# Kernel optimization log

Measured on AMD Instinct MI355X. Metric: run time of the kernel, lower is better.

The kernel has to match this reference:

```python
import jax, jax.numpy as jnp
import numpy as np

N, E, IN, HID, HEADS, LAYERS, CLASSES = 50000, 800000, 256, 128, 4, 3, 2
DH = HID // HEADS
EPS = 1e-5


def _layernorm(h, g, b):
    mu = jnp.mean(h, axis=-1, keepdims=True)
    var = jnp.mean(jnp.square(h - mu), axis=-1, keepdims=True)
    return (h - mu) / jnp.sqrt(var + EPS) * g + b


def setup_inputs() -> dict:
    key = jax.random.key(0)
    ks = jax.random.split(key, 16)

    def w(k, shape, fan_in):
        return jax.random.normal(k, shape, dtype=jnp.float32) / np.sqrt(fan_in).astype(np.float32)

    inp = {}
    inp["x"] = jax.random.normal(ks[0], (N, IN), dtype=jnp.float32)
    inp["edge_index"] = jax.random.randint(ks[1], (2, E), 0, N, dtype=jnp.int32)
    inp["batch"] = jnp.zeros((N,), dtype=jnp.int32)  # single graph
    # feature extractor: Linear(IN,HID) -> ReLU -> Linear(HID,HID)
    inp["fe_w1"] = w(ks[2], (HID, IN), IN)
    inp["fe_b1"] = jnp.zeros((HID,), jnp.float32)
    inp["fe_w2"] = w(ks[3], (HID, HID), HID)
    inp["fe_b2"] = jnp.zeros((HID,), jnp.float32)
    inp["conv_w"] = w(ks[4], (LAYERS, HID, 2 * HID), 2 * HID)
    inp["conv_b"] = jnp.zeros((LAYERS, HID), jnp.float32)
    inp["ln_g"] = jnp.ones((LAYERS, HID), jnp.float32)
    inp["ln_b"] = jnp.zeros((LAYERS, HID), jnp.float32)
    # MultiheadAttention(HID, 4 heads): packed in_proj + out_proj
    inp["in_proj_w"] = w(ks[5], (3 * HID, HID), HID)
    inp["in_proj_b"] = jnp.zeros((3 * HID,), jnp.float32)
    inp["out_w"] = w(ks[6], (HID, HID), HID)
    inp["out_b"] = jnp.zeros((HID,), jnp.float32)
    # classifier: Linear(2*HID, HID) -> ReLU -> Linear(HID, CLASSES)
    inp["c_w1"] = w(ks[7], (HID, 2 * HID), 2 * HID)
    inp["c_b1"] = jnp.zeros((HID,), jnp.float32)
    inp["c_w2"] = w(ks[8], (CLASSES, HID), HID)
    inp["c_b2"] = jnp.zeros((CLASSES,), jnp.float32)
    return inp


def reference(x, edge_index, batch, fe_w1, fe_b1, fe_w2, fe_b2, conv_w, conv_b,
              ln_g, ln_b, in_proj_w, in_proj_b, out_w, out_b, c_w1, c_b1, c_w2, c_b2):
    # feature extractor (dropout inactive in eval mode)
    h = jax.nn.relu(x @ fe_w1.T + fe_b1) @ fe_w2.T + fe_b2  # [N, HID]
    row, col = edge_index[0], edge_index[1]
    for i in range(LAYERS):
        # scatter_add of source-node features onto destination nodes
        nbr = jax.ops.segment_sum(h[row], col, num_segments=N)  # [N, HID]
        hcat = jnp.concatenate([h, nbr], axis=-1)               # [N, 2*HID]
        h = _layernorm(hcat @ conv_w[i].T + conv_b[i], ln_g[i], ln_b[i])
        h = jax.nn.relu(h)
    # MultiheadAttention with h.unsqueeze(0) and batch_first=False:
    # seq_len = 1, batch = N -> softmax over a single key yields weight 1.
    qkv = h @ in_proj_w.T + in_proj_b                          # [N, 3*HID]
    q, k, v = jnp.split(qkv, 3, axis=-1)
    qh = q.reshape(N, HEADS, DH)
    kh = k.reshape(N, HEADS, DH)
    vh = v.reshape(N, HEADS, DH)
    scores = jnp.sum(qh * kh, axis=-1) / np.sqrt(DH).astype(np.float32)  # [N, H]
    wts = jax.nn.softmax(scores[..., None], axis=-1)           # [N, H, 1] == 1
    attn = wts * vh                                            # [N, H, DH]
    h_attn = attn.reshape(N, HID) @ out_w.T + out_b
    h = h + h_attn
    # global mean / max pool over (all-zero) batch ids
    counts = jax.ops.segment_sum(jnp.ones((N, 1), h.dtype), batch, num_segments=1)
    h_mean = jax.ops.segment_sum(h, batch, num_segments=1) / counts      # [1, HID]
    h_max = jax.ops.segment_max(h, batch, num_segments=1)                # [1, HID]
    g = jnp.concatenate([h_mean, h_max], axis=-1)                        # [1, 2*HID]
    return jax.nn.relu(g @ c_w1.T + c_b1) @ c_w2.T + c_b2                # [1, CLASSES]
```

## Files before the change

kernel.cpp:

```cpp
#include <hip/hip_runtime.h>

constexpr int HID = 128;
constexpr int SCHUNK = 1024;
constexpr int CPAD = 16;

typedef __attribute__((ext_vector_type(8))) short short8;
typedef __attribute__((ext_vector_type(8))) unsigned short us8;
typedef __attribute__((ext_vector_type(4))) unsigned short us4;
typedef __attribute__((ext_vector_type(4))) float f32x4;

__device__ __forceinline__ unsigned short f2bf(float f) {
    union { float f; unsigned u; } v; v.f = f;
    unsigned r = v.u + 0x7fffu + ((v.u >> 16) & 1u);
    return (unsigned short)(r >> 16);
}
__device__ __forceinline__ float bf2f(unsigned short u) {
    union { unsigned u; float f; } v; v.u = ((unsigned)u) << 16;
    return v.f;
}

template<int K, bool CONCAT, bool AF32, bool RELU, bool LN>
__device__ __forceinline__
void mgemm_body(int bid, const unsigned short* __restrict__ A1b,
                const float* __restrict__ A1f, const unsigned short* __restrict__ A2b,
                const unsigned short* __restrict__ Wb, const float* __restrict__ bias,
                const float* __restrict__ lng, const float* __restrict__ lnb,
                unsigned short* __restrict__ C, int nrows)
{
    constexpr int LDT = 40;
    __shared__ unsigned short As[128 * LDT];
    __shared__ unsigned short Ws[128 * LDT];
    const int tid = threadIdx.x;
    const int w = tid >> 6, l = tid & 63;
    const int lr = l & 15, lg = l >> 4;
    const int row0 = bid * 128;

    f32x4 acc[2][8] = {};

    const int sr = tid >> 1;
    const int sc = (tid & 1) * 16;

    int gr = row0 + sr; if (gr >= nrows) gr = nrows - 1;

    for (int k0 = 0; k0 < K; k0 += 32) {
        us8 a0, a1;
        if (AF32) {
            const float* fsrc = A1f + (size_t)gr * K + k0 + sc;
            float4 f0 = *(const float4*)(fsrc + 0);
            float4 f1 = *(const float4*)(fsrc + 4);
            float4 f2 = *(const float4*)(fsrc + 8);
            float4 f3 = *(const float4*)(fsrc + 12);
            a0[0]=f2bf(f0.x); a0[1]=f2bf(f0.y); a0[2]=f2bf(f0.z); a0[3]=f2bf(f0.w);
            a0[4]=f2bf(f1.x); a0[5]=f2bf(f1.y); a0[6]=f2bf(f1.z); a0[7]=f2bf(f1.w);
            a1[0]=f2bf(f2.x); a1[1]=f2bf(f2.y); a1[2]=f2bf(f2.z); a1[3]=f2bf(f2.w);
            a1[4]=f2bf(f3.x); a1[5]=f2bf(f3.y); a1[6]=f2bf(f3.z); a1[7]=f2bf(f3.w);
        } else {
            const unsigned short* bsrc;
            if (CONCAT) bsrc = ((k0 < 128) ? A1b : A2b) + (size_t)gr * 128 + (k0 & 127) + sc;
            else        bsrc = A1b + (size_t)gr * K + k0 + sc;
            a0 = *(const us8*)(bsrc + 0);
            a1 = *(const us8*)(bsrc + 8);
        }
        *(us8*)&As[sr * LDT + sc + 0] = a0;
        *(us8*)&As[sr * LDT + sc + 8] = a1;

        {
            const unsigned short* s = Wb + (size_t)sr * K + k0 + sc;
            *(us8*)&Ws[sr * LDT + sc + 0] = *(const us8*)(s + 0);
            *(us8*)&Ws[sr * LDT + sc + 8] = *(const us8*)(s + 8);
        }
        __syncthreads();

        short8 afr[2];
#pragma unroll
        for (int rt = 0; rt < 2; rt++)
            afr[rt] = *(const short8*)&As[(w * 32 + rt * 16 + lr) * LDT + lg * 8];
#pragma unroll
        for (int ct = 0; ct < 8; ct++) {
            short8 bfr = *(const short8*)&Ws[(ct * 16 + lr) * LDT + lg * 8];
#pragma unroll
            for (int rt = 0; rt < 2; rt++)
                acc[rt][ct] = __builtin_amdgcn_mfma_f32_16x16x32_bf16(
                    afr[rt], bfr, acc[rt][ct], 0, 0, 0);
        }
        __syncthreads();
    }

    float bia[8], g8[8], be[8];
#pragma unroll
    for (int ct = 0; ct < 8; ct++) {
        bia[ct] = bias[ct * 16 + lr];
        if (LN) { g8[ct] = lng[ct * 16 + lr]; be[ct] = lnb[ct * 16 + lr]; }
    }
#pragma unroll
    for (int rt = 0; rt < 2; rt++) {
#pragma unroll
        for (int r_ = 0; r_ < 4; r_++) {
            int row = row0 + w * 32 + rt * 16 + lg * 4 + r_;
            float v[8];
#pragma unroll
            for (int ct = 0; ct < 8; ct++) v[ct] = acc[rt][ct][r_] + bia[ct];
            if (LN) {
                float s = 0.f;
#pragma unroll
                for (int ct = 0; ct < 8; ct++) s += v[ct];
#pragma unroll
                for (int m = 8; m >= 1; m >>= 1) s += __shfl_xor(s, m);
                float mean = s * (1.f / 128.f);
                float q = 0.f;
#pragma unroll
                for (int ct = 0; ct < 8; ct++) { v[ct] -= mean; q += v[ct] * v[ct]; }
#pragma unroll
                for (int m = 8; m >= 1; m >>= 1) q += __shfl_xor(q, m);
                float rstd = rsqrtf(q * (1.f / 128.f) + 1e-5f);
#pragma unroll
                for (int ct = 0; ct < 8; ct++) v[ct] = v[ct] * rstd * g8[ct] + be[ct];
            }
            if (RELU) {
#pragma unroll
                for (int ct = 0; ct < 8; ct++) v[ct] = fmaxf(v[ct], 0.f);
            }
            if (row < nrows) {
#pragma unroll
                for (int ct = 0; ct < 8; ct++)
                    C[(size_t)row * 128 + ct * 16 + lr] = f2bf(v[ct]);
            }
        }
    }
}

template<int K, bool CONCAT, bool AF32, bool RELU, bool LN>
__global__ __launch_bounds__(256)
void mgemm(const unsigned short* __restrict__ A1b, const float* __restrict__ A1f,
           const unsigned short* __restrict__ A2b, const unsigned short* __restrict__ Wb,
           const float* __restrict__ bias, const float* __restrict__ lng,
           const float* __restrict__ lnb, unsigned short* __restrict__ C, int nrows)
{
    mgemm_body<K,CONCAT,AF32,RELU,LN>(blockIdx.x, A1b, A1f, A2b, Wb, bias, lng, lnb, C, nrows);
}

__device__ __forceinline__ void cvt_blk(const float* __restrict__ src,
                                        unsigned short* __restrict__ dst,
                                        int relb, int n)
{
    int i = (relb * 256 + threadIdx.x) * 4;
    if (i < n) {
        float4 v = *(const float4*)(src + i);
        us4 o; o[0]=f2bf(v.x); o[1]=f2bf(v.y); o[2]=f2bf(v.z); o[3]=f2bf(v.w);
        *(us4*)(dst + i) = o;
    }
}

__global__ __launch_bounds__(256)
void prep(const float* __restrict__ fe_w1, unsigned short* __restrict__ w1b,
          const float* __restrict__ fe_w2, unsigned short* __restrict__ w2b,
          const float* __restrict__ conv_w, unsigned short* __restrict__ cwb,
          const float* __restrict__ out_w, const float* __restrict__ v_w,
          const float* __restrict__ out_b, const float* __restrict__ bv,
          unsigned short* __restrict__ Mb, float* __restrict__ bias2,
          const int* __restrict__ ecol, int* __restrict__ degp, int E)
{
    const int b = blockIdx.x;
    const int tid = threadIdx.x;
    constexpr int B1 = 32, B2 = B1 + 16, B3 = B2 + 96, B4 = B3 + 64;
    if (b < B1) {
        cvt_blk(fe_w1, w1b, b, 128*256);
    } else if (b < B2) {
        cvt_blk(fe_w2, w2b, b - B1, 128*128);
    } else if (b < B3) {
        cvt_blk(conv_w, cwb, b - B2, 3*128*256);
    } else if (b < B4) {
        const int i = (b - B3) * 2 + (tid >> 7);
        const int j = tid & 127;
        float s = 0.f;
        for (int k = 0; k < 128; k++)
            s = fmaf(out_w[i*128 + k], v_w[k*128 + j], s);
        Mb[i*128 + j] = f2bf(s + ((i == j) ? 1.f : 0.f));
        if (j == 0) {
            float bb = out_b[i];
            for (int k = 0; k < 128; k++)
                bb = fmaf(out_w[i*128 + k], bv[k], bb);
            bias2[i] = bb;
        }
    } else {
        int e = (b - B4) * 256 + tid;
        if (e < E) atomicAdd(&degp[(size_t)ecol[e] * CPAD], 1);
    }
}

__global__ __launch_bounds__(256)
void scan_chunk(const int* __restrict__ degp, int* __restrict__ off,
                int* __restrict__ bsum, int n)
{
    __shared__ int wsum[4];
    const int t = threadIdx.x;
    const int base = blockIdx.x * SCHUNK + t * 4;
    int v[4];
#pragma unroll
    for (int j = 0; j < 4; j++) v[j] = (base + j < n) ? degp[(size_t)(base + j) * CPAD] : 0;
    int tsum = v[0] + v[1] + v[2] + v[3];
    int inc = tsum;
#pragma unroll
    for (int d2 = 1; d2 < 64; d2 <<= 1) {
        int u = __shfl_up(inc, d2);
        if ((t & 63) >= d2) inc += u;
    }
    if ((t & 63) == 63) wsum[t >> 6] = inc;
    __syncthreads();
    int woff = 0;
#pragma unroll
    for (int w = 0; w < 4; w++) if (w < (t >> 6)) woff += wsum[w];
    int ex = woff + inc - tsum;
#pragma unroll
    for (int j = 0; j < 4; j++) {
        if (base + j < n) off[base + j] = ex;
        ex += v[j];
    }
    if (t == 255) bsum[blockIdx.x] = woff + inc;
}

__global__ void scan_bsum(int* bsum, int nblk)
{
    if (threadIdx.x == 0 && blockIdx.x == 0) {
        int run = 0;
        for (int b = 0; b < nblk; b++) { int x = bsum[b]; bsum[b] = run; run += x; }
    }
}

__global__ __launch_bounds__(256)
void scan_add(int* __restrict__ off, int* __restrict__ cursorp,
              const int* __restrict__ bsum, int n)
{
    int i = blockIdx.x * 256 + threadIdx.x;
    if (i < n) {
        int o = off[i] + bsum[i >> 10];
        off[i] = o;
        cursorp[(size_t)i * CPAD] = o;
    }
}

__global__ __launch_bounds__(256)
void fe1_csr(const float* __restrict__ x, const unsigned short* __restrict__ w1b,
             const float* __restrict__ fe_b1, unsigned short* __restrict__ outh,
             int nrows, int gb,
             const int* __restrict__ erow, const int* __restrict__ ecol,
             int* __restrict__ cursorp, int* __restrict__ csr, int E)
{
    const int b = blockIdx.x;
    if (b < gb) {
        mgemm_body<256,false,true,true,false>(b, nullptr, x, nullptr, w1b, fe_b1,
                                              nullptr, nullptr, outh, nrows);
    } else {
        int e = (b - gb) * 256 + threadIdx.x;
        if (e < E) {
            int c = ecol[e];
            int p = atomicAdd(&cursorp[(size_t)c * CPAD], 1);
            csr[p] = erow[e];
        }
    }
}

__global__ __launch_bounds__(256)
void gather_sum(const unsigned short* __restrict__ h, const int* __restrict__ off,
                const int* __restrict__ degp, const int* __restrict__ csr,
                unsigned short* __restrict__ nbr, int N)
{
    int gw = (blockIdx.x * 256 + threadIdx.x) >> 6;
    if (gw >= N) return;
    const int lane = threadIdx.x & 63;
    const int start = off[gw];
    const int d = degp[(size_t)gw * CPAD];
    const unsigned* hp = (const unsigned*)h + lane;
    float ax[8] = {}, ay[8] = {};
    int i = 0;
    for (; i + 8 <= d; i += 8) {
        int s[8];
#pragma unroll
        for (int j = 0; j < 8; j++) s[j] = csr[start + i + j];
        unsigned u[8];
#pragma unroll
        for (int j = 0; j < 8; j++) u[j] = hp[(size_t)s[j] * 64];
#pragma unroll
        for (int j = 0; j < 8; j++) {
            ax[j] += __uint_as_float(u[j] << 16);
            ay[j] += __uint_as_float(u[j] & 0xffff0000u);
        }
    }
    for (; i < d; i++) {
        unsigned u = hp[(size_t)csr[start + i] * 64];
        ax[0] += __uint_as_float(u << 16);
        ay[0] += __uint_as_float(u & 0xffff0000u);
    }
    float sx = ((ax[0]+ax[1]) + (ax[2]+ax[3])) + ((ax[4]+ax[5]) + (ax[6]+ax[7]));
    float sy = ((ay[0]+ay[1]) + (ay[2]+ay[3])) + ((ay[4]+ay[5]) + (ay[6]+ay[7]));
    unsigned o = ((unsigned)f2bf(sx)) | (((unsigned)f2bf(sy)) << 16);
    *((unsigned*)nbr + (size_t)gw * 64 + lane) = o;
}

__global__ __launch_bounds__(256)
void pool_partial(const unsigned short* __restrict__ h, float* __restrict__ part, int n)
{
    const int tid = threadIdx.x;
    const int col = tid & 127;
    const int sub = tid >> 7;
    float s = 0.f, m = -3.402823466e+38f;
    for (int r = blockIdx.x*2 + sub; r < n; r += gridDim.x*2) {
        float v = bf2f(h[(size_t)r*HID + col]);
        s += v;
        m = fmaxf(m, v);
    }
    __shared__ float ls[2][128], lm[2][128];
    ls[sub][col] = s; lm[sub][col] = m;
    __syncthreads();
    if (sub == 0) {
        s += ls[1][col];
        m = fmaxf(m, lm[1][col]);
        part[blockIdx.x*256 + col]       = s;
        part[blockIdx.x*256 + 128 + col] = m;
    }
}

__global__ __launch_bounds__(256)
void pool_reduce16(const float* __restrict__ part, float* __restrict__ part2,
                   int nblocks)
{
    const int t = threadIdx.x;
    const int b0 = blockIdx.x;
    if (t < 128) {
        float s = 0.f;
        for (int b = b0; b < nblocks; b += 16) s += part[b*256 + t];
        part2[b0*256 + t] = s;
    } else {
        float m = -3.402823466e+38f;
        for (int b = b0; b < nblocks; b += 16) m = fmaxf(m, part[b*256 + t]);
        part2[b0*256 + t] = m;
    }
}

__global__ __launch_bounds__(256)
void cls_fused(const float* __restrict__ part2, int n,
               const float* __restrict__ cw1, const float* __restrict__ cb1,
               const float* __restrict__ cw2, const float* __restrict__ cb2,
               float* __restrict__ out, int classes)
{
    __shared__ float g[256];
    __shared__ float t1[128];
    const int tid = threadIdx.x;
    if (tid < 128) {
        float s = 0.f;
#pragma unroll
        for (int b = 0; b < 16; b++) s += part2[b*256 + tid];
        g[tid] = s / (float)n;
    } else {
        float m = -3.402823466e+38f;
#pragma unroll
        for (int b = 0; b < 16; b++) m = fmaxf(m, part2[b*256 + tid]);
        g[tid] = m;
    }
    __syncthreads();
    const int w = tid >> 6, lane = tid & 63;
    float4 gv = *(const float4*)&g[lane*4];
#pragma unroll 4
    for (int i = 0; i < 32; i++) {
        int r = w * 32 + i;
        float4 wv = *(const float4*)(cw1 + (size_t)r*256 + lane*4);
        float p = wv.x*gv.x + wv.y*gv.y + wv.z*gv.z + wv.w*gv.w;
#pragma unroll
        for (int m = 32; m >= 1; m >>= 1) p += __shfl_xor(p, m);
        if (lane == 0) t1[r] = fmaxf(p + cb1[r], 0.f);
    }
    __syncthreads();
    if (tid < 128) {
        int c = tid >> 6;
        if (c < classes) {
            float p = t1[lane] * cw2[c*128 + lane] + t1[lane+64] * cw2[c*128 + lane + 64];
#pragma unroll
            for (int m = 32; m >= 1; m >>= 1) p += __shfl_xor(p, m);
            if (lane == 0) out[c] = p + cb2[c];
        }
    }
}

extern "C" void kernel_launch(void* const* d_in, const int* in_sizes, int n_in,
                              void* d_out, int out_size, void* d_ws, size_t ws_size,
                              hipStream_t stream)
{
    const float* x        = (const float*)d_in[0];
    const int*   ei       = (const int*)  d_in[1];
    const float* fe_w1    = (const float*)d_in[3];
    const float* fe_b1    = (const float*)d_in[4];
    const float* fe_w2    = (const float*)d_in[5];
    const float* fe_b2    = (const float*)d_in[6];
    const float* conv_w   = (const float*)d_in[7];
    const float* conv_b   = (const float*)d_in[8];
    const float* ln_g     = (const float*)d_in[9];
    const float* ln_b     = (const float*)d_in[10];
    const float* in_proj_w= (const float*)d_in[11];
    const float* in_proj_b= (const float*)d_in[12];
    const float* out_w    = (const float*)d_in[13];
    const float* out_b    = (const float*)d_in[14];
    const float* c_w1     = (const float*)d_in[15];
    const float* c_b1     = (const float*)d_in[16];
    const float* c_w2     = (const float*)d_in[17];
    const float* c_b2     = (const float*)d_in[18];
    float* out = (float*)d_out;

    const int N = in_sizes[0] / 256;
    const int E = in_sizes[1] / 2;
    const int CLASSES = out_size;
    const int* erow = ei;
    const int* ecol = ei + E;

    const size_t NH = (size_t)N * HID;

    unsigned short* nbrb  = (unsigned short*)d_ws;
    unsigned short* hb0   = nbrb + NH;
    unsigned short* hb1   = hb0 + NH;
    float*          part  = (float*)(hb1 + NH);
    float*          part2 = part + 512*256;
    float*          bias2 = part2 + 16*256;
    unsigned short* w1b   = (unsigned short*)(bias2 + 128);
    unsigned short* w2b   = w1b + 128*256;
    unsigned short* cwb   = w2b + 128*128;
    unsigned short* Mb    = cwb + 3*128*256;
    int*            degp  = (int*)(Mb + 128*128);
    int*            cursorp = degp + (size_t)N * CPAD;
    int*            off   = cursorp + (size_t)N * CPAD;
    int*            csr   = off + N;
    int*            bsum  = csr + E;

    const int gblocks = (N + 127) / 128;
    const int eblocks = (E + 255) / 256;
    const int nchunk  = (N + SCHUNK - 1) / SCHUNK;
    dim3 blk(256);

    hipMemsetAsync(degp, 0, (size_t)N * CPAD * sizeof(int), stream);
    prep<<<32 + 16 + 96 + 64 + eblocks, blk, 0, stream>>>(
        fe_w1, w1b, fe_w2, w2b, conv_w, cwb,
        out_w, in_proj_w + (size_t)2*HID*HID, out_b, in_proj_b + 2*HID,
        Mb, bias2, ecol, degp, E);

    scan_chunk<<<nchunk, blk, 0, stream>>>(degp, off, bsum, N);
    scan_bsum<<<1, 64, 0, stream>>>(bsum, nchunk);
    scan_add<<<(N + 255) / 256, blk, 0, stream>>>(off, cursorp, bsum, N);

    fe1_csr<<<gblocks + eblocks, blk, 0, stream>>>(
        x, w1b, fe_b1, hb1, N, gblocks, erow, ecol, cursorp, csr, E);

    mgemm<128,false,false,false,false><<<gblocks, blk, 0, stream>>>(
        hb1, nullptr, nullptr, w2b, fe_b2, nullptr, nullptr, hb0, N);

    unsigned short* h = hb0;
    unsigned short* other = hb1;
    const int wblocks = (int)(((size_t)N * 64 + 255) / 256);
    for (int l = 0; l < 3; l++) {
        gather_sum<<<wblocks, blk, 0, stream>>>(h, off, degp, csr, nbrb, N);
        mgemm<256,true ,false,true ,true ><<<gblocks, blk, 0, stream>>>(
            h, nullptr, nbrb, cwb + (size_t)l*128*256, conv_b + l*HID,
            ln_g + l*HID, ln_b + l*HID, other, N);
        unsigned short* t = h; h = other; other = t;
    }

    unsigned short* hf = other;
    mgemm<128,false,false,false,false><<<gblocks, blk, 0, stream>>>(
        h, nullptr, nullptr, Mb, bias2, nullptr, nullptr, hf, N);

    const int PB = 512;
    pool_partial<<<PB, blk, 0, stream>>>(hf, part, N);
    pool_reduce16<<<16, blk, 0, stream>>>(part, part2, PB);
    cls_fused<<<1, blk, 0, stream>>>(part2, N, c_w1, c_b1, c_w2, c_b2, out, CLASSES);
}
```

Measured before the change: 317.8 us.

## Fuse fe1 GEMM into prep, fe2 into CSR build, and pooling into final GEMM

The first feature-extractor GEMM now reads fp32 weights directly and runs inside the prep kernel alongside the weight conversion and degree counting. The second feature-extractor GEMM is moved into the CSR-fill kernel, and the final attention GEMM computes per-block sum/max pool partials in its epilogue instead of writing the output and launching a separate pool kernel. This removes two launches and one full N×HID write and read-back. In exchange, fe1 converts weights on the fly from fp32 and the GEMM epilogue gains an extra LDS reduction.

```diff
diff --git a/kernel.cpp b/kernel.cpp
--- a/kernel.cpp
+++ b/kernel.cpp
@@ -19,17 +19,30 @@
     return v.f;
 }
 
-template<int K, bool CONCAT, bool AF32, bool RELU, bool LN>
+__device__ __forceinline__ void ld16f_bf(const float* s, us8& o0, us8& o1) {
+    float4 f0 = *(const float4*)(s + 0);
+    float4 f1 = *(const float4*)(s + 4);
+    float4 f2 = *(const float4*)(s + 8);
+    float4 f3 = *(const float4*)(s + 12);
+    o0[0]=f2bf(f0.x); o0[1]=f2bf(f0.y); o0[2]=f2bf(f0.z); o0[3]=f2bf(f0.w);
+    o0[4]=f2bf(f1.x); o0[5]=f2bf(f1.y); o0[6]=f2bf(f1.z); o0[7]=f2bf(f1.w);
+    o1[0]=f2bf(f2.x); o1[1]=f2bf(f2.y); o1[2]=f2bf(f2.z); o1[3]=f2bf(f2.w);
+    o1[4]=f2bf(f3.x); o1[5]=f2bf(f3.y); o1[6]=f2bf(f3.z); o1[7]=f2bf(f3.w);
+}
+
+template<int K, bool CONCAT, bool AF32, bool RELU, bool LN, bool WF32, bool POOL>
 __device__ __forceinline__
 void mgemm_body(int bid, const unsigned short* __restrict__ A1b,
                 const float* __restrict__ A1f, const unsigned short* __restrict__ A2b,
-                const unsigned short* __restrict__ Wb, const float* __restrict__ bias,
-                const float* __restrict__ lng, const float* __restrict__ lnb,
-                unsigned short* __restrict__ C, int nrows)
+                const unsigned short* __restrict__ Wb, const float* __restrict__ Wf,
+                const float* __restrict__ bias, const float* __restrict__ lng,
+                const float* __restrict__ lnb, unsigned short* __restrict__ C,
+                float* __restrict__ part, int nrows)
 {
     constexpr int LDT = 40;
-    __shared__ unsigned short As[128 * LDT];
-    __shared__ unsigned short Ws[128 * LDT];
+    __shared__ unsigned short lds[2 * 128 * LDT];
+    unsigned short* As = lds;
+    unsigned short* Ws = lds + 128 * LDT;
     const int tid = threadIdx.x;
     const int w = tid >> 6, l = tid & 63;
     const int lr = l & 15, lg = l >> 4;
@@ -45,15 +58,7 @@
     for (int k0 = 0; k0 < K; k0 += 32) {
         us8 a0, a1;
         if (AF32) {
-            const float* fsrc = A1f + (size_t)gr * K + k0 + sc;
-            float4 f0 = *(const float4*)(fsrc + 0);
-            float4 f1 = *(const float4*)(fsrc + 4);
-            float4 f2 = *(const float4*)(fsrc + 8);
-            float4 f3 = *(const float4*)(fsrc + 12);
-            a0[0]=f2bf(f0.x); a0[1]=f2bf(f0.y); a0[2]=f2bf(f0.z); a0[3]=f2bf(f0.w);
-            a0[4]=f2bf(f1.x); a0[5]=f2bf(f1.y); a0[6]=f2bf(f1.z); a0[7]=f2bf(f1.w);
-            a1[0]=f2bf(f2.x); a1[1]=f2bf(f2.y); a1[2]=f2bf(f2.z); a1[3]=f2bf(f2.w);
-            a1[4]=f2bf(f3.x); a1[5]=f2bf(f3.y); a1[6]=f2bf(f3.z); a1[7]=f2bf(f3.w);
+            ld16f_bf(A1f + (size_t)gr * K + k0 + sc, a0, a1);
         } else {
             const unsigned short* bsrc;
             if (CONCAT) bsrc = ((k0 < 128) ? A1b : A2b) + (size_t)gr * 128 + (k0 & 127) + sc;
@@ -64,11 +69,16 @@
         *(us8*)&As[sr * LDT + sc + 0] = a0;
         *(us8*)&As[sr * LDT + sc + 8] = a1;
 
-        {
+        us8 b0, b1;
+        if (WF32) {
+            ld16f_bf(Wf + (size_t)sr * K + k0 + sc, b0, b1);
+        } else {
             const unsigned short* s = Wb + (size_t)sr * K + k0 + sc;
-            *(us8*)&Ws[sr * LDT + sc + 0] = *(const us8*)(s + 0);
-            *(us8*)&Ws[sr * LDT + sc + 8] = *(const us8*)(s + 8);
-        }
+            b0 = *(const us8*)(s + 0);
+            b1 = *(const us8*)(s + 8);
+        }
+        *(us8*)&Ws[sr * LDT + sc + 0] = b0;
+        *(us8*)&Ws[sr * LDT + sc + 8] = b1;
         __syncthreads();
 
         short8 afr[2];
@@ -92,6 +102,11 @@
         bia[ct] = bias[ct * 16 + lr];
         if (LN) { g8[ct] = lng[ct * 16 + lr]; be[ct] = lnb[ct * 16 + lr]; }
     }
+    float ps[8], pm[8];
+    if (POOL) {
+#pragma unroll
+        for (int ct = 0; ct < 8; ct++) { ps[ct] = 0.f; pm[ct] = -3.402823466e+38f; }
+    }
 #pragma unroll
     for (int rt = 0; rt < 2; rt++) {
 #pragma unroll
@@ -121,22 +136,53 @@
                 for (int ct = 0; ct < 8; ct++) v[ct] = fmaxf(v[ct], 0.f);
             }
             if (row < nrows) {
-#pragma unroll
-                for (int ct = 0; ct < 8; ct++)
-                    C[(size_t)row * 128 + ct * 16 + lr] = f2bf(v[ct]);
+                if (POOL) {
+#pragma unroll
+                    for (int ct = 0; ct < 8; ct++) {
+                        ps[ct] += v[ct];
+                        pm[ct] = fmaxf(pm[ct], v[ct]);
+                    }
+                } else {
+#pragma unroll
+                    for (int ct = 0; ct < 8; ct++)
+                        C[(size_t)row * 128 + ct * 16 + lr] = f2bf(v[ct]);
+                }
             }
         }
     }
-}
-
-template<int K, bool CONCAT, bool AF32, bool RELU, bool LN>
+    if (POOL) {
+        float* scr = (float*)lds;
+        const int g = w * 4 + lg;
+#pragma unroll
+        for (int ct = 0; ct < 8; ct++) {
+            int col = ct * 16 + lr;
+            scr[g * 128 + col] = ps[ct];
+            scr[2048 + g * 128 + col] = pm[ct];
+        }
+        __syncthreads();
+        if (tid < 128) {
+            float s = 0.f, m = -3.402823466e+38f;
+#pragma unroll
+            for (int gg = 0; gg < 16; gg++) {
+                s += scr[gg * 128 + tid];
+                m = fmaxf(m, scr[2048 + gg * 128 + tid]);
+            }
+            part[bid * 256 + tid] = s;
+            part[bid * 256 + 128 + tid] = m;
+        }
+    }
+}
+
+template<int K, bool CONCAT, bool AF32, bool RELU, bool LN, bool WF32, bool POOL>
 __global__ __launch_bounds__(256)
 void mgemm(const unsigned short* __restrict__ A1b, const float* __restrict__ A1f,
            const unsigned short* __restrict__ A2b, const unsigned short* __restrict__ Wb,
-           const float* __restrict__ bias, const float* __restrict__ lng,
-           const float* __restrict__ lnb, unsigned short* __restrict__ C, int nrows)
-{
-    mgemm_body<K,CONCAT,AF32,RELU,LN>(blockIdx.x, A1b, A1f, A2b, Wb, bias, lng, lnb, C, nrows);
+           const float* __restrict__ Wf, const float* __restrict__ bias,
+           const float* __restrict__ lng, const float* __restrict__ lnb,
+           unsigned short* __restrict__ C, float* __restrict__ part, int nrows)
+{
+    mgemm_body<K,CONCAT,AF32,RELU,LN,WF32,POOL>(blockIdx.x, A1b, A1f, A2b, Wb, Wf,
+                                                bias, lng, lnb, C, part, nrows);
 }
 
 __device__ __forceinline__ void cvt_blk(const float* __restrict__ src,
@@ -152,25 +198,31 @@
 }
 
 __global__ __launch_bounds__(256)
-void prep(const float* __restrict__ fe_w1, unsigned short* __restrict__ w1b,
-          const float* __restrict__ fe_w2, unsigned short* __restrict__ w2b,
-          const float* __restrict__ conv_w, unsigned short* __restrict__ cwb,
-          const float* __restrict__ out_w, const float* __restrict__ v_w,
-          const float* __restrict__ out_b, const float* __restrict__ bv,
-          unsigned short* __restrict__ Mb, float* __restrict__ bias2,
-          const int* __restrict__ ecol, int* __restrict__ degp, int E)
+void fe1_prep(const float* __restrict__ x, const float* __restrict__ fe_w1,
+              const float* __restrict__ fe_b1, unsigned short* __restrict__ outh,
+              int nrows, int gb,
+              const float* __restrict__ fe_w2, unsigned short* __restrict__ w2b,
+              const float* __restrict__ conv_w, unsigned short* __restrict__ cwb,
+              const float* __restrict__ out_w, const float* __restrict__ v_w,
+              const float* __restrict__ out_b, const float* __restrict__ bv,
+              unsigned short* __restrict__ Mb, float* __restrict__ bias2,
+              const int* __restrict__ ecol, int* __restrict__ degp, int E)
 {
     const int b = blockIdx.x;
     const int tid = threadIdx.x;
-    constexpr int B1 = 32, B2 = B1 + 16, B3 = B2 + 96, B4 = B3 + 64;
-    if (b < B1) {
-        cvt_blk(fe_w1, w1b, b, 128*256);
-    } else if (b < B2) {
-        cvt_blk(fe_w2, w2b, b - B1, 128*128);
-    } else if (b < B3) {
-        cvt_blk(conv_w, cwb, b - B2, 3*128*256);
-    } else if (b < B4) {
-        const int i = (b - B3) * 2 + (tid >> 7);
+    if (b < gb) {
+        mgemm_body<256,false,true,true,false,true,false>(
+            b, nullptr, x, nullptr, nullptr, fe_w1, fe_b1, nullptr, nullptr,
+            outh, nullptr, nrows);
+        return;
+    }
+    const int b2 = b - gb;
+    if (b2 < 16) {
+        cvt_blk(fe_w2, w2b, b2, 128*128);
+    } else if (b2 < 112) {
+        cvt_blk(conv_w, cwb, b2 - 16, 3*128*256);
+    } else if (b2 < 176) {
+        const int i = (b2 - 112) * 2 + (tid >> 7);
         const int j = tid & 127;
         float s = 0.f;
         for (int k = 0; k < 128; k++)
@@ -183,7 +235,7 @@
             bias2[i] = bb;
         }
     } else {
-        int e = (b - B4) * 256 + tid;
+        int e = (b2 - 176) * 256 + tid;
         if (e < E) atomicAdd(&degp[(size_t)ecol[e] * CPAD], 1);
     }
 }
@@ -240,16 +292,17 @@
 }
 
 __global__ __launch_bounds__(256)
-void fe1_csr(const float* __restrict__ x, const unsigned short* __restrict__ w1b,
-             const float* __restrict__ fe_b1, unsigned short* __restrict__ outh,
+void fe2_csr(const unsigned short* __restrict__ hin, const unsigned short* __restrict__ w2b,
+             const float* __restrict__ fe_b2, unsigned short* __restrict__ outh,
              int nrows, int gb,
              const int* __restrict__ erow, const int* __restrict__ ecol,
              int* __restrict__ cursorp, int* __restrict__ csr, int E)
 {
     const int b = blockIdx.x;
     if (b < gb) {
-        mgemm_body<256,false,true,true,false>(b, nullptr, x, nullptr, w1b, fe_b1,
-                                              nullptr, nullptr, outh, nrows);
+        mgemm_body<128,false,false,false,false,false,false>(
+            b, hin, nullptr, nullptr, w2b, nullptr, fe_b2, nullptr, nullptr,
+            outh, nullptr, nrows);
     } else {
         int e = (b - gb) * 256 + threadIdx.x;
         if (e < E) {
@@ -295,29 +348,6 @@
     float sy = ((ay[0]+ay[1]) + (ay[2]+ay[3])) + ((ay[4]+ay[5]) + (ay[6]+ay[7]));
     unsigned o = ((unsigned)f2bf(sx)) | (((unsigned)f2bf(sy)) << 16);
     *((unsigned*)nbr + (size_t)gw * 64 + lane) = o;
-}
-
-__global__ __launch_bounds__(256)
-void pool_partial(const unsigned short* __restrict__ h, float* __restrict__ part, int n)
-{
-    const int tid = threadIdx.x;
-    const int col = tid & 127;
-    const int sub = tid >> 7;
-    float s = 0.f, m = -3.402823466e+38f;
-    for (int r = blockIdx.x*2 + sub; r < n; r += gridDim.x*2) {
-        float v = bf2f(h[(size_t)r*HID + col]);
-        s += v;
-        m = fmaxf(m, v);
-    }
-    __shared__ float ls[2][128], lm[2][128];
-    ls[sub][col] = s; lm[sub][col] = m;
-    __syncthreads();
-    if (sub == 0) {
-        s += ls[1][col];
-        m = fmaxf(m, lm[1][col]);
-        part[blockIdx.x*256 + col]       = s;
-        part[blockIdx.x*256 + 128 + col] = m;
-    }
 }
 
 __global__ __launch_bounds__(256)
@@ -419,8 +449,7 @@
     float*          part  = (float*)(hb1 + NH);
     float*          part2 = part + 512*256;
     float*          bias2 = part2 + 16*256;
-    unsigned short* w1b   = (unsigned short*)(bias2 + 128);
-    unsigned short* w2b   = w1b + 128*256;
+    unsigned short* w2b   = (unsigned short*)(bias2 + 128);
     unsigned short* cwb   = w2b + 128*128;
     unsigned short* Mb    = cwb + 3*128*256;
     int*            degp  = (int*)(Mb + 128*128);
@@ -435,8 +464,9 @@
     dim3 blk(256);
 
     hipMemsetAsync(degp, 0, (size_t)N * CPAD * sizeof(int), stream);
-    prep<<<32 + 16 + 96 + 64 + eblocks, blk, 0, stream>>>(
-        fe_w1, w1b, fe_w2, w2b, conv_w, cwb,
+    fe1_prep<<<gblocks + 176 + eblocks, blk, 0, stream>>>(
+        x, fe_w1, fe_b1, hb1, N, gblocks,
+        fe_w2, w2b, conv_w, cwb,
         out_w, in_proj_w + (size_t)2*HID*HID, out_b, in_proj_b + 2*HID,
         Mb, bias2, ecol, degp, E);
 
@@ -444,29 +474,24 @@
     scan_bsum<<<1, 64, 0, stream>>>(bsum, nchunk);
     scan_add<<<(N + 255) / 256, blk, 0, stream>>>(off, cursorp, bsum, N);
 
-    fe1_csr<<<gblocks + eblocks, blk, 0, stream>>>(
-        x, w1b, fe_b1, hb1, N, gblocks, erow, ecol, cursorp, csr, E);
-
-    mgemm<128,false,false,false,false><<<gblocks, blk, 0, stream>>>(
-        hb1, nullptr, nullptr, w2b, fe_b2, nullptr, nullptr, hb0, N);
+    fe2_csr<<<gblocks + eblocks, blk, 0, stream>>>(
+        hb1, w2b, fe_b2, hb0, N, gblocks, erow, ecol, cursorp, csr, E);
 
     unsigned short* h = hb0;
     unsigned short* other = hb1;
     const int wblocks = (int)(((size_t)N * 64 + 255) / 256);
     for (int l = 0; l < 3; l++) {
         gather_sum<<<wblocks, blk, 0, stream>>>(h, off, degp, csr, nbrb, N);
-        mgemm<256,true ,false,true ,true ><<<gblocks, blk, 0, stream>>>(
-            h, nullptr, nbrb, cwb + (size_t)l*128*256, conv_b + l*HID,
-            ln_g + l*HID, ln_b + l*HID, other, N);
+        mgemm<256,true,false,true,true,false,false><<<gblocks, blk, 0, stream>>>(
+            h, nullptr, nbrb, cwb + (size_t)l*128*256, nullptr, conv_b + l*HID,
+            ln_g + l*HID, ln_b + l*HID, other, nullptr, N);
         unsigned short* t = h; h = other; other = t;
     }
 
-    unsigned short* hf = other;
-    mgemm<128,false,false,false,false><<<gblocks, blk, 0, stream>>>(
-        h, nullptr, nullptr, Mb, bias2, nullptr, nullptr, hf, N);
-
-    const int PB = 512;
-    pool_partial<<<PB, blk, 0, stream>>>(hf, part, N);
-    pool_reduce16<<<16, blk, 0, stream>>>(part, part2, PB);
+    mgemm<128,false,false,false,false,false,true><<<gblocks, blk, 0, stream>>>(
+        h, nullptr, nullptr, Mb, nullptr, bias2, nullptr, nullptr,
+        nullptr, part, N);
+
+    pool_reduce16<<<16, blk, 0, stream>>>(part, part2, gblocks);
     cls_fused<<<1, blk, 0, stream>>>(part2, N, c_w1, c_b1, c_w2, c_b2, out, CLASSES);
 }
```

Result: faster. 303.3 us (-4.6%).
